# Optimization experiments

Measured on AMD Instinct MI355X. Metric: run time of the kernel, lower is better.

## Reference

```python
import jax, jax.numpy as jnp
import numpy as np

B, TOPK, E, C, K = 64, 2, 16, 1024, 4096


def setup_inputs() -> dict:
    key = jax.random.key(0)
    k1, k2, k3, k4, k5, k6 = jax.random.split(key, 6)
    return {
        "activated": jax.random.normal(k1, (B, TOPK, K), dtype=jnp.float32),
        "expert_indices": jax.random.randint(k2, (B, TOPK), 0, E, dtype=jnp.int64)
        if jax.config.jax_enable_x64 else jax.random.randint(k2, (B, TOPK), 0, E, dtype=jnp.int32),
        "expert_weights": jax.random.uniform(k3, (B, TOPK), dtype=jnp.float32),
        "mlp2_weight": jax.random.normal(k4, (E, C, K), dtype=jnp.float32),
        "mlp2_bias": jax.random.normal(k5, (E, C), dtype=jnp.float32),
        "residual_x": jax.random.normal(k6, (B, C), dtype=jnp.float32),
    }


def reference(activated, expert_indices, expert_weights, mlp2_weight, mlp2_bias, residual_x):
    # Gather per-token expert weights/biases: w [B, topk, C, K], b [B, topk, C]
    w = mlp2_weight[expert_indices]
    b = mlp2_bias[expert_indices]
    # Batched matvec per (token, expert slot): t [B, topk, C]
    t = jnp.einsum("beck,bek->bec", w, activated) + b
    # Weighted combine over top-k expert slots, plus residual: [B, C]
    return residual_x + jnp.einsum("bec,be->bc", t, expert_weights)
```

## Files before the change

kernel.cpp:

```cpp
#include <hip/hip_runtime.h>

#define BB    64
#define TOPK  2
#define EE    16
#define CC    1024
#define KK    4096

constexpr int RPB = 16;
constexpr int P   = 16;
constexpr int KS  = 8;
constexpr int KH  = KK / KS;
constexpr int NW  = KH / 4 / 64;

typedef float v4f __attribute__((ext_vector_type(4)));

__global__ __launch_bounds__(256, 4) void moe_mlp2(
    const float* __restrict__ act, const int* __restrict__ idx,
    const float* __restrict__ W, float* __restrict__ partial)
{
    __shared__ float sact[P][KH];
    __shared__ int   slist[BB * TOPK];
    __shared__ int   scnt;

    const int bid  = blockIdx.x;
    const int e    = bid >> 9;
    const int ct   = (bid >> 3) & 63;
    const int ks   = bid & (KS - 1);
    const int tid  = threadIdx.x;
    const int lane = tid & 63;
    const int wave = tid >> 6;
    const int row0 = ct * RPB + wave * 4;

    if (tid == 0) scnt = 0;
    __syncthreads();
    if (tid < BB * TOPK && idx[tid] == e) {
        int pos = atomicAdd(&scnt, 1);
        slist[pos] = tid;
    }
    __syncthreads();
    const int n = scnt;
    if (n == 0) return;

    const v4f* __restrict__ Wb =
        (const v4f*)(W + (size_t)(e * CC + row0) * KK + ks * KH);
    v4f w[4][NW];
#pragma unroll
    for (int r = 0; r < 4; r++)
#pragma unroll
        for (int kw = 0; kw < NW; kw++)
            w[r][kw] = __builtin_nontemporal_load(
                Wb + (size_t)r * (KK / 4) + kw * 64 + lane);

    for (int g = 0; g < n; g += P) {
        const int np = min(P, n - g);
        if (g) __syncthreads();

        for (int h = wave; h < 2 * np; h += 4) {
            int pr = slist[g + (h >> 1)];
            const float* gsrc = act + (size_t)pr * KK + ks * KH
                              + (h & 1) * (KH / 2) + lane * 4;
            __builtin_amdgcn_global_load_lds(
                (const __attribute__((address_space(1))) void*)gsrc,
                (__attribute__((address_space(3))) void*)
                    &sact[h >> 1][(h & 1) * (KH / 2)],
                16, 0, 0);
        }
        __syncthreads();

        float val[64];
#pragma unroll
        for (int i = 0; i < 64; i++) val[i] = 0.f;

#pragma unroll
        for (int kw = 0; kw < NW; kw++) {
            const int fb = (kw * 64 + lane) * 4;
#pragma unroll
            for (int pc = 0; pc < P / 4; pc++) {
                if (pc * 4 < np) {
#pragma unroll
                    for (int j = 0; j < 4; j++) {
                        const int p = pc * 4 + j;
                        const v4f a = *(const v4f*)&sact[p][fb];
#pragma unroll
                        for (int r = 0; r < 4; r++)
                            val[(p << 2) | r] +=
                                w[r][kw].x * a.x + w[r][kw].y * a.y +
                                w[r][kw].z * a.z + w[r][kw].w * a.w;
                    }
                }
            }
        }

#pragma unroll
        for (int s = 0; s < 6; s++) {
            const int m = 1 << s;
            const bool hi = (lane & m) != 0;
#pragma unroll
            for (int i = 0; i < 64; i += 2 * m) {
                float send = hi ? val[i] : val[i + m];
                float recv = __shfl_xor(send, m, 64);
                val[i] = (hi ? val[i + m] : val[i]) + recv;
            }
        }

        const int p = lane >> 2;
        if (p < np) {
            int pr = slist[g + p];
            partial[((size_t)pr * KS + ks) * CC + row0 + (lane & 3)] = val[0];
        }
    }
}

__global__ __launch_bounds__(256) void finalize(
    const int* __restrict__ idx, const float* __restrict__ ew,
    const float* __restrict__ bias, const float* __restrict__ resid,
    const float* __restrict__ partial, float* __restrict__ out)
{
    const int i = blockIdx.x * 256 + threadIdx.x;
    const int b = i >> 10;
    const int c = i & (CC - 1);
    float v = resid[i];
#pragma unroll
    for (int s = 0; s < TOPK; s++) {
        const int pr = b * TOPK + s;
        const int e  = idx[pr];
        float t = bias[e * CC + c];
#pragma unroll
        for (int ks = 0; ks < KS; ks++)
            t += partial[((size_t)pr * KS + ks) * CC + c];
        v += ew[pr] * t;
    }
    out[i] = v;
}

extern "C" void kernel_launch(void* const* d_in, const int* in_sizes, int n_in,
                              void* d_out, int out_size, void* d_ws, size_t ws_size,
                              hipStream_t stream) {
    const float* act   = (const float*)d_in[0];
    const int*   idx   = (const int*)d_in[1];
    const float* ew    = (const float*)d_in[2];
    const float* W     = (const float*)d_in[3];
    const float* bias  = (const float*)d_in[4];
    const float* resid = (const float*)d_in[5];
    float* out = (float*)d_out;

    float* partial = (float*)d_ws;

    moe_mlp2<<<EE * 64 * KS, 256, 0, stream>>>(act, idx, W, partial);
    finalize<<<(BB * CC) / 256, 256, 0, stream>>>(
        idx, ew, bias, resid, partial, out);
}
```

Measured before the change: 354.7 us.

## Overlap first activation staging with weight loads and shorten small-group reduction

Issues the first group's activation global-to-LDS loads before the per-thread weight loads, then uses a partial vmcnt wait and a raw barrier so the activation staging overlaps the weight fetch latency. The weight register array is reordered by k-chunk so the partial wait covers the chunks needed first. When a group has at most eight pairs, a shorter 5-step shuffle reduction over 32 values plus one extra xor is used instead of the full 6-step tree. The hand-written waitcnt and barrier rely on the exact load issue order, and the compiler could reorder loads around them.

Measured after the change: 351.5 us (median of 2 runs). No clear change (-0.9%).

```diff
diff --git a/kernel.cpp b/kernel.cpp
--- a/kernel.cpp
+++ b/kernel.cpp
@@ -43,18 +43,8 @@
 
     const v4f* __restrict__ Wb =
         (const v4f*)(W + (size_t)(e * CC + row0) * KK + ks * KH);
-    v4f w[4][NW];
-#pragma unroll
-    for (int r = 0; r < 4; r++)
-#pragma unroll
-        for (int kw = 0; kw < NW; kw++)
-            w[r][kw] = __builtin_nontemporal_load(
-                Wb + (size_t)r * (KK / 4) + kw * 64 + lane);
 
-    for (int g = 0; g < n; g += P) {
-        const int np = min(P, n - g);
-        if (g) __syncthreads();
-
+    auto STAGE = [&](int g, int np) {
         for (int h = wave; h < 2 * np; h += 4) {
             int pr = slist[g + (h >> 1)];
             const float* gsrc = act + (size_t)pr * KK + ks * KH
@@ -65,7 +55,33 @@
                     &sact[h >> 1][(h & 1) * (KH / 2)],
                 16, 0, 0);
         }
-        __syncthreads();
+    };
+
+    v4f w[NW][4];
+    {
+        const int np0 = min(P, n);
+        STAGE(0, np0);
+        __builtin_amdgcn_sched_barrier(0);
+#pragma unroll
+        for (int kw = 0; kw < NW; kw++)
+#pragma unroll
+            for (int r = 0; r < 4; r++)
+                w[kw][r] = __builtin_nontemporal_load(
+                    Wb + (size_t)r * (KK / 4) + kw * 64 + lane);
+        __builtin_amdgcn_sched_barrier(0);
+        asm volatile("s_waitcnt vmcnt(8)" ::: "memory");
+        __builtin_amdgcn_sched_barrier(0);
+        __builtin_amdgcn_s_barrier();
+        __builtin_amdgcn_sched_barrier(0);
+    }
+
+    for (int g = 0; g < n; g += P) {
+        const int np = min(P, n - g);
+        if (g) {
+            __syncthreads();
+            STAGE(g, np);
+            __syncthreads();
+        }
 
         float val[64];
 #pragma unroll
@@ -84,29 +100,50 @@
 #pragma unroll
                         for (int r = 0; r < 4; r++)
                             val[(p << 2) | r] +=
-                                w[r][kw].x * a.x + w[r][kw].y * a.y +
-                                w[r][kw].z * a.z + w[r][kw].w * a.w;
+                                w[kw][r].x * a.x + w[kw][r].y * a.y +
+                                w[kw][r].z * a.z + w[kw][r].w * a.w;
                     }
                 }
             }
         }
 
+        if (np <= 8) {
 #pragma unroll
-        for (int s = 0; s < 6; s++) {
-            const int m = 1 << s;
-            const bool hi = (lane & m) != 0;
+            for (int s = 0; s < 5; s++) {
+                const int m = 1 << s;
+                const bool hi = (lane & m) != 0;
 #pragma unroll
-            for (int i = 0; i < 64; i += 2 * m) {
-                float send = hi ? val[i] : val[i + m];
-                float recv = __shfl_xor(send, m, 64);
-                val[i] = (hi ? val[i + m] : val[i]) + recv;
+                for (int i = 0; i < 32; i += 2 * m) {
+                    float send = hi ? val[i] : val[i + m];
+                    float recv = __shfl_xor(send, m, 64);
+                    val[i] = (hi ? val[i + m] : val[i]) + recv;
+                }
             }
-        }
-
-        const int p = lane >> 2;
-        if (p < np) {
-            int pr = slist[g + p];
-            partial[((size_t)pr * KS + ks) * CC + row0 + (lane & 3)] = val[0];
+            float v0 = val[0];
+            v0 += __shfl_xor(v0, 32, 64);
+            const int p = (lane & 31) >> 2;
+            if (lane < 32 && p < np) {
+                int pr = slist[g + p];
+                partial[((size_t)pr * KS + ks) * CC + row0 + (lane & 3)] = v0;
+            }
+        } else {
+#pragma unroll
+            for (int s = 0; s < 6; s++) {
+                const int m = 1 << s;
+                const bool hi = (lane & m) != 0;
+#pragma unroll
+                for (int i = 0; i < 64; i += 2 * m) {
+                    float send = hi ? val[i] : val[i + m];
+                    float recv = __shfl_xor(send, m, 64);
+                    val[i] = (hi ? val[i + m] : val[i]) + recv;
+                }
+            }
+            const int p = lane >> 2;
+            if (p < np) {
+                int pr = slist[g + p];
+                partial[((size_t)pr * KS + ks) * CC + row0 + (lane & 3)] =
+                    val[0];
+            }
         }
     }
 }
```
